# Kernel tuning notes

Measured on AMD Instinct MI355X. Metric: run time of the kernel, lower is better.

## Reference

```python
import jax, jax.numpy as jnp
import numpy as np

POOL = 4      # pool_size
SR = 2        # sampling_ratio (fixed; torchvision adaptive default approximated)
C_IN = 1024
C1, C2 = 256, 128
OUT_DIM = 2048


def setup_inputs() -> dict:
    key = jax.random.key(0)
    ks = jax.random.split(key, 10)
    B, C, H, W = 8, C_IN, 64, 64
    N = 64
    x = jax.random.normal(ks[0], (B, C, H, W), dtype=jnp.float32)
    # boxes in image pixel coords (image is H*16 = 1024 px)
    img = 1024.0
    x1 = jax.random.uniform(ks[1], (B, N), minval=0.0, maxval=img - 260.0)
    y1 = jax.random.uniform(ks[2], (B, N), minval=0.0, maxval=img - 260.0)
    bw = jax.random.uniform(ks[3], (B, N), minval=32.0, maxval=256.0)
    bh = jax.random.uniform(ks[4], (B, N), minval=32.0, maxval=256.0)
    boxes = jnp.stack([x1, y1, x1 + bw, y1 + bh], axis=-1)  # [B,N,4]
    scale = jnp.float32(1.0 / 16.0)
    # detector params
    w1 = jax.random.normal(ks[5], (C1, C_IN), dtype=jnp.float32) / np.sqrt(C_IN)
    b1 = jnp.zeros((C1,), dtype=jnp.float32)
    w2 = jax.random.normal(ks[6], (C2, C1), dtype=jnp.float32) / np.sqrt(C1)
    b2 = jnp.zeros((C2,), dtype=jnp.float32)
    wl = jax.random.normal(ks[7], (OUT_DIM, C2 * POOL * POOL), dtype=jnp.float32) / np.sqrt(C2 * POOL * POOL)
    bl = jnp.zeros((OUT_DIM,), dtype=jnp.float32)
    return {"x": x, "boxes": boxes, "scale": scale,
            "w1": w1, "b1": b1, "w2": w2, "b2": b2, "wl": wl, "bl": bl}


def _axis_coords(start, size, H):
    # start,size: [R]; returns coords [R, POOL*SR], valid mask, int low/high, lerp wts
    bin_sz = size / POOL                       # [R]
    j = jnp.arange(POOL * SR, dtype=jnp.float32)
    off = jnp.floor(j / SR) + ((j % SR) + 0.5) / SR   # [P]
    c = start[:, None] + off[None, :] * bin_sz[:, None]  # [R,P]
    valid = (c >= -1.0) & (c <= H)
    c = jnp.clip(c, 0.0, H - 1.0)
    lo = jnp.floor(c).astype(jnp.int32)
    lo = jnp.minimum(lo, H - 1)
    hi = jnp.minimum(lo + 1, H - 1)
    frac = c - lo.astype(c.dtype)
    return valid, lo, hi, frac


def _roi_align(feat, boxes, scale):
    # feat: [B,C,H,W], boxes: [B,N,4] -> pooled [B*N, C, POOL, POOL]
    B, C, H, W = feat.shape
    N = boxes.shape[1]
    R = B * N
    bx = (boxes.reshape(R, 4) * scale)
    x1, y1, x2, y2 = bx[:, 0], bx[:, 1], bx[:, 2], bx[:, 3]
    rw = jnp.maximum(x2 - x1, 1.0)
    rh = jnp.maximum(y2 - y1, 1.0)
    vy, y_lo, y_hi, ly = _axis_coords(y1, rh, H)   # [R,P]
    vx, x_lo, x_hi, lx = _axis_coords(x1, rw, W)
    hy, hx = 1.0 - ly, 1.0 - lx
    bidx = jnp.repeat(jnp.arange(B, dtype=jnp.int32), N)  # [R]
    b = bidx[:, None, None]
    # gather 4 corners -> [R,P,P,C]
    v00 = feat[b, :, y_lo[:, :, None], x_lo[:, None, :]]
    v01 = feat[b, :, y_lo[:, :, None], x_hi[:, None, :]]
    v10 = feat[b, :, y_hi[:, :, None], x_lo[:, None, :]]
    v11 = feat[b, :, y_hi[:, :, None], x_hi[:, None, :]]
    w00 = (hy[:, :, None] * hx[:, None, :])[..., None]
    w01 = (hy[:, :, None] * lx[:, None, :])[..., None]
    w10 = (ly[:, :, None] * hx[:, None, :])[..., None]
    w11 = (ly[:, :, None] * lx[:, None, :])[..., None]
    val = v00 * w00 + v01 * w01 + v10 * w10 + v11 * w11
    mask = (vy[:, :, None] & vx[:, None, :])[..., None]
    val = jnp.where(mask, val, 0.0)            # [R,P,P,C]
    val = val.reshape(R, POOL, SR, POOL, SR, C).mean(axis=(2, 4))  # [R,POOL,POOL,C]
    return jnp.transpose(val, (0, 3, 1, 2))    # [R,C,POOL,POOL]


def reference(x, boxes, scale, w1, b1, w2, b2, wl, bl):
    pooled = _roi_align(x, boxes, scale)                  # [R,C,4,4]
    h = jax.nn.elu(jnp.einsum('rchw,oc->rohw', pooled, w1) + b1[None, :, None, None])
    h = jax.nn.elu(jnp.einsum('rchw,oc->rohw', h, w2) + b2[None, :, None, None])
    h = h.reshape(h.shape[0], -1)                         # [R, 128*16], torch Flatten order
    out = jax.nn.elu(h @ wl.T + bl)                       # [R, 2048]
    return out
```

## Files before the change

kernel.cpp:

```cpp
#include <hip/hip_runtime.h>
#include <math.h>

#define C_INK   1024
#define C1D     256
#define C2D     128
#define OUTD    2048
#define R_ROI   512
#define M1D     8192
#define MPIX    32768

typedef _Float16 half8 __attribute__((ext_vector_type(8)));
typedef float    f32x4 __attribute__((ext_vector_type(4)));

__device__ __forceinline__ unsigned int pack2h(float a, float b) {
    union { _Float16 h[2]; unsigned int u; } p;
    p.h[0] = (_Float16)a; p.h[1] = (_Float16)b;
    return p.u;
}
__device__ __forceinline__ float eluf(float v) { return v > 0.f ? v : expf(v) - 1.f; }

template<int RC>
__device__ __forceinline__ half8* ldsq(_Float16* base, int row, int ch) {
    return reinterpret_cast<half8*>(base) + row * RC + (ch ^ (row & 7));
}

__global__ __launch_bounds__(256) void cvt_weights(
    const float* __restrict__ s1, _Float16* __restrict__ d1, int n1,
    const float* __restrict__ s2, _Float16* __restrict__ d2, int n2,
    const float* __restrict__ s3, _Float16* __restrict__ d3, int n3)
{
    int i = (blockIdx.x * 256 + threadIdx.x) * 4;
    const float* s; _Float16* d;
    if (i < n1)            { s = s1; d = d1; }
    else if (i < n1 + n2)  { s = s2; d = d2; i -= n1; }
    else                   { s = s3; d = d3; i -= n1 + n2; if (i >= n3) return; }
    const float4 v = *reinterpret_cast<const float4*>(s + i);
    uint2 u; u.x = pack2h(v.x, v.y); u.y = pack2h(v.z, v.w);
    *reinterpret_cast<uint2*>(d + i) = u;
}

__global__ __launch_bounds__(512, 4) void conv1x1_f16(
    const float* __restrict__ x, const _Float16* __restrict__ w1h,
    _Float16* __restrict__ z)
{
    __shared__ __align__(16) _Float16 As[64 * 64];
    __shared__ __align__(16) _Float16 Bs[256 * 64];

    const int tid  = threadIdx.x;
    const int lane = tid & 63;
    const int wave = tid >> 6;
    const int m0   = blockIdx.x * 64;
    const int b    = m0 >> 12;
    const int p0   = m0 & 4095;

    const int bc  = tid & 7;
    const int br0 = tid >> 3;

    float ar[8];
    half8 brg[4];
    f32x4 acc[4][2];
    #pragma unroll
    for (int i = 0; i < 4; ++i)
        #pragma unroll
        for (int j = 0; j < 2; ++j) acc[i][j] = (f32x4){0.f, 0.f, 0.f, 0.f};

    const float* xbase = x + (size_t)b * C_INK * 4096 + p0 + lane;

    auto LOADT = [&](int k0) {
        const float* xk = xbase + (size_t)(k0 + wave * 8) * 4096;
        #pragma unroll
        for (int j = 0; j < 8; ++j) ar[j] = xk[(size_t)j * 4096];
        #pragma unroll
        for (int i = 0; i < 4; ++i)
            brg[i] = *reinterpret_cast<const half8*>(
                &w1h[(size_t)(br0 + i * 64) * C_INK + k0 + bc * 8]);
    };
    auto WRITET = [&]() {
        union { half8 h; unsigned int u[4]; } pk;
        #pragma unroll
        for (int j = 0; j < 4; ++j) pk.u[j] = pack2h(ar[2 * j], ar[2 * j + 1]);
        *ldsq<8>(As, lane, wave) = pk.h;
        #pragma unroll
        for (int i = 0; i < 4; ++i) *ldsq<8>(Bs, br0 + i * 64, bc) = brg[i];
    };
    auto COMPUTET = [&]() {
        #pragma unroll
        for (int kk = 0; kk < 2; ++kk) {
            const int ch = kk * 4 + (lane >> 4);
            half8 af[4], bf[2];
            #pragma unroll
            for (int mi = 0; mi < 4; ++mi) af[mi] = *ldsq<8>(As, mi * 16 + (lane & 15), ch);
            #pragma unroll
            for (int ni = 0; ni < 2; ++ni) bf[ni] = *ldsq<8>(Bs, wave * 32 + ni * 16 + (lane & 15), ch);
            #pragma unroll
            for (int mi = 0; mi < 4; ++mi)
                #pragma unroll
                for (int ni = 0; ni < 2; ++ni)
                    acc[mi][ni] = __builtin_amdgcn_mfma_f32_16x16x32_f16(af[mi], bf[ni], acc[mi][ni], 0, 0, 0);
        }
    };

    LOADT(0); WRITET(); __syncthreads();
    for (int t = 0; t < 15; ++t) {
        LOADT((t + 1) * 64);
        COMPUTET();
        __syncthreads();
        WRITET();
        __syncthreads();
    }
    COMPUTET();

    _Float16* zp = z + (size_t)m0 * C1D;
    #pragma unroll
    for (int mi = 0; mi < 4; ++mi)
        #pragma unroll
        for (int ni = 0; ni < 2; ++ni)
            #pragma unroll
            for (int j = 0; j < 4; ++j) {
                const int row = mi * 16 + (lane >> 4) * 4 + j;
                const int col = wave * 32 + ni * 16 + (lane & 15);
                zp[(size_t)row * C1D + col] = (_Float16)acc[mi][ni][j];
            }
}

__global__ __launch_bounds__(256) void roi_gemm2_f16(
    const _Float16* __restrict__ z, const float* __restrict__ boxes,
    const float* __restrict__ scale_p, const float* __restrict__ b1v,
    const _Float16* __restrict__ w2h, const float* __restrict__ b2v,
    _Float16* __restrict__ h2)
{
    __shared__ __align__(16) _Float16 W2s[128 * 256];
    __shared__ __align__(16) _Float16 H1s[16 * 256];
    __shared__ int   s_off[64][4];
    __shared__ float s_w[64][4];

    const int r    = blockIdx.x;
    const int tid  = threadIdx.x;
    const int lane = tid & 63;

    if (tid < 64) {
        const float sc = scale_p[0];
        const float x1 = boxes[r * 4 + 0] * sc, y1 = boxes[r * 4 + 1] * sc;
        const float x2 = boxes[r * 4 + 2] * sc, y2 = boxes[r * 4 + 3] * sc;
        const float rw = fmaxf(x2 - x1, 1.f), rh = fmaxf(y2 - y1, 1.f);
        const int jy = tid >> 3, jx = tid & 7;

        float offy = (float)(jy >> 1) + (float)(jy & 1) * 0.5f + 0.25f;
        float cy = y1 + offy * rh * 0.25f;
        const bool vy = (cy >= -1.f) && (cy <= 64.f);
        cy = fminf(fmaxf(cy, 0.f), 63.f);
        int ylo = (int)cy; if (ylo > 63) ylo = 63;
        int yhi = ylo + 1; if (yhi > 63) yhi = 63;
        const float ly = cy - (float)ylo, hy = 1.f - ly;

        float offx = (float)(jx >> 1) + (float)(jx & 1) * 0.5f + 0.25f;
        float cx = x1 + offx * rw * 0.25f;
        const bool vx = (cx >= -1.f) && (cx <= 64.f);
        cx = fminf(fmaxf(cx, 0.f), 63.f);
        int xlo = (int)cx; if (xlo > 63) xlo = 63;
        int xhi = xlo + 1; if (xhi > 63) xhi = 63;
        const float lx = cx - (float)xlo, hx = 1.f - lx;

        const float wm = (vy && vx) ? 0.25f : 0.f;
        s_w[tid][0] = hy * hx * wm;
        s_w[tid][1] = hy * lx * wm;
        s_w[tid][2] = ly * hx * wm;
        s_w[tid][3] = ly * lx * wm;
        s_off[tid][0] = (ylo * 64 + xlo) * C1D;
        s_off[tid][1] = (ylo * 64 + xhi) * C1D;
        s_off[tid][2] = (yhi * 64 + xlo) * C1D;
        s_off[tid][3] = (yhi * 64 + xhi) * C1D;
    }

    {
        const int wr_ = tid >> 1;
        const int wcb = (tid & 1) * 16;
        #pragma unroll
        for (int bb = 0; bb < 4; ++bb) {
            half8 tmp[4];
            #pragma unroll
            for (int i = 0; i < 4; ++i)
                tmp[i] = *reinterpret_cast<const half8*>(&w2h[(size_t)wr_ * C1D + (wcb + bb * 4 + i) * 8]);
            #pragma unroll
            for (int i = 0; i < 4; ++i)
                *ldsq<32>(W2s, wr_, wcb + bb * 4 + i) = tmp[i];
        }
    }
    __syncthreads();

    {
        const int ch8 = tid & 31;
        const int cg  = tid >> 5;
        const _Float16* zb = z + (size_t)(r >> 6) * 4096 * C1D + ch8 * 8;

        float bias[8];
        {
            const float4 b0 = *reinterpret_cast<const float4*>(&b1v[ch8 * 8]);
            const float4 b4 = *reinterpret_cast<const float4*>(&b1v[ch8 * 8 + 4]);
            bias[0] = b0.x; bias[1] = b0.y; bias[2] = b0.z; bias[3] = b0.w;
            bias[4] = b4.x; bias[5] = b4.y; bias[6] = b4.z; bias[7] = b4.w;
        }

        float accv[2][8];
        #pragma unroll
        for (int c = 0; c < 2; ++c)
            #pragma unroll
            for (int e = 0; e < 8; ++e) accv[c][e] = 0.f;

        #pragma unroll
        for (int cc = 0; cc < 2; ++cc) {
            const int cell = cg * 2 + cc;
            const int py = cell >> 2, px = cell & 3;
            #pragma unroll
            for (int u = 0; u < 4; ++u) {
                const int s = (py * 2 + (u >> 1)) * 8 + px * 2 + (u & 1);
                #pragma unroll
                for (int k = 0; k < 4; ++k) {
                    const half8 v = *reinterpret_cast<const half8*>(zb + s_off[s][k]);
                    const float w = s_w[s][k];
                    #pragma unroll
                    for (int e = 0; e < 8; ++e) accv[cc][e] += (float)v[e] * w;
                }
            }
        }

        #pragma unroll
        for (int cc = 0; cc < 2; ++cc) {
            half8 o;
            #pragma unroll
            for (int e = 0; e < 8; ++e) o[e] = (_Float16)eluf(accv[cc][e] + bias[e]);
            *ldsq<32>(H1s, cg * 2 + cc, ch8) = o;
        }
    }
    __syncthreads();

    {
        const int wv = tid >> 6;
        f32x4 o2[2];
        o2[0] = (f32x4){0.f, 0.f, 0.f, 0.f};
        o2[1] = (f32x4){0.f, 0.f, 0.f, 0.f};

        #pragma unroll
        for (int ks = 0; ks < 8; ++ks) {
            const int ch = ks * 4 + (lane >> 4);
            const half8 af = *ldsq<32>(H1s, lane & 15, ch);
            #pragma unroll
            for (int i = 0; i < 2; ++i) {
                const half8 bf = *ldsq<32>(W2s, (wv * 2 + i) * 16 + (lane & 15), ch);
                o2[i] = __builtin_amdgcn_mfma_f32_16x16x32_f16(af, bf, o2[i], 0, 0, 0);
            }
        }

        _Float16* hp = h2 + (size_t)r * 2048;
        #pragma unroll
        for (int i = 0; i < 2; ++i) {
            const int o = (wv * 2 + i) * 16 + (lane & 15);
            const float bv = b2v[o];
            #pragma unroll
            for (int j = 0; j < 4; ++j) {
                const int p = (lane >> 4) * 4 + j;
                hp[o * 16 + p] = (_Float16)eluf(o2[i][j] + bv);
            }
        }
    }
}

template<int BM, int FM>
__global__ __launch_bounds__(256) void gemm_nt(
    const _Float16* __restrict__ A, const _Float16* __restrict__ W,
    const float* __restrict__ bias, float* __restrict__ Cout, int K, int N)
{
    constexpr int WM = FM * 16;
    constexpr int AI = BM / 32;
    __shared__ __align__(16) _Float16 As[BM * 64];
    __shared__ __align__(16) _Float16 Bs[128 * 64];

    const int tid  = threadIdx.x;
    const int lane = tid & 63;
    const int wave = tid >> 6;
    const int wr   = wave >> 1, wc = wave & 1;
    const int m0   = blockIdx.x * BM;
    const int n0   = blockIdx.y * 128;
    const int c    = tid & 7;
    const int r0   = tid >> 3;

    half8 arg[AI], brg[4];
    f32x4 acc[FM][4];
    #pragma unroll
    for (int i = 0; i < FM; ++i)
        #pragma unroll
        for (int j = 0; j < 4; ++j) acc[i][j] = (f32x4){0.f, 0.f, 0.f, 0.f};

    auto LOADT = [&](int k0) {
        #pragma unroll
        for (int i = 0; i < AI; ++i)
            arg[i] = *reinterpret_cast<const half8*>(&A[(size_t)(m0 + r0 + i * 32) * K + k0 + c * 8]);
        #pragma unroll
        for (int i = 0; i < 4; ++i)
            brg[i] = *reinterpret_cast<const half8*>(&W[(size_t)(n0 + r0 + i * 32) * K + k0 + c * 8]);
    };
    auto WRITET = [&]() {
        #pragma unroll
        for (int i = 0; i < AI; ++i) *ldsq<8>(As, r0 + i * 32, c) = arg[i];
        #pragma unroll
        for (int i = 0; i < 4; ++i)  *ldsq<8>(Bs, r0 + i * 32, c) = brg[i];
    };
    auto COMPUTET = [&]() {
        #pragma unroll
        for (int kk = 0; kk < 2; ++kk) {
            const int ch = kk * 4 + (lane >> 4);
            half8 af[FM], bf[4];
            #pragma unroll
            for (int mi = 0; mi < FM; ++mi) af[mi] = *ldsq<8>(As, wr * WM + mi * 16 + (lane & 15), ch);
            #pragma unroll
            for (int ni = 0; ni < 4; ++ni)  bf[ni] = *ldsq<8>(Bs, wc * 64 + ni * 16 + (lane & 15), ch);
            #pragma unroll
            for (int mi = 0; mi < FM; ++mi)
                #pragma unroll
                for (int ni = 0; ni < 4; ++ni)
                    acc[mi][ni] = __builtin_amdgcn_mfma_f32_16x16x32_f16(af[mi], bf[ni], acc[mi][ni], 0, 0, 0);
        }
    };

    const int nt = K / 64;
    LOADT(0); WRITET(); __syncthreads();
    for (int t = 0; t < nt - 1; ++t) {
        LOADT((t + 1) * 64);
        COMPUTET();
        __syncthreads();
        WRITET();
        __syncthreads();
    }
    COMPUTET();

    #pragma unroll
    for (int ni = 0; ni < 4; ++ni) {
        const int col = n0 + wc * 64 + ni * 16 + (lane & 15);
        const float bv = bias[col];
        #pragma unroll
        for (int mi = 0; mi < FM; ++mi)
            #pragma unroll
            for (int j = 0; j < 4; ++j) {
                const int row = m0 + wr * WM + mi * 16 + (lane >> 4) * 4 + j;
                Cout[(size_t)row * N + col] = eluf(acc[mi][ni][j] + bv);
            }
    }
}

extern "C" void kernel_launch(void* const* d_in, const int* in_sizes, int n_in,
                              void* d_out, int out_size, void* d_ws, size_t ws_size,
                              hipStream_t stream) {
    const float* x     = (const float*)d_in[0];
    const float* boxes = (const float*)d_in[1];
    const float* scale = (const float*)d_in[2];
    const float* w1    = (const float*)d_in[3];
    const float* b1    = (const float*)d_in[4];
    const float* w2    = (const float*)d_in[5];
    const float* b2    = (const float*)d_in[6];
    const float* wl    = (const float*)d_in[7];
    const float* bl    = (const float*)d_in[8];
    float* out = (float*)d_out;

    _Float16* z   = (_Float16*)d_ws;
    _Float16* h2  = z   + (size_t)MPIX * C1D;
    _Float16* w1h = h2  + (size_t)R_ROI * OUTD;
    _Float16* w2h = w1h + (size_t)C1D * C_INK;
    _Float16* wlh = w2h + (size_t)C2D * C1D;

    const int n1 = C1D * C_INK, n2 = C2D * C1D, n3 = OUTD * OUTD;

    cvt_weights<<<dim3((n1 + n2 + n3) / 1024), dim3(256), 0, stream>>>(
        w1, w1h, n1, w2, w2h, n2, wl, wlh, n3);

    conv1x1_f16<<<dim3(MPIX / 64), dim3(512), 0, stream>>>(x, w1h, z);

    roi_gemm2_f16<<<dim3(R_ROI), dim3(256), 0, stream>>>(
        z, boxes, scale, b1, w2h, b2, h2);

    gemm_nt<64, 2><<<dim3(R_ROI / 64, OUTD / 128), dim3(256), 0, stream>>>(
        h2, wlh, bl, out, OUTD, OUTD);
}
```

Measured before the change: 80.64 us.

## Restructure ROI and output GEMM kernels with 512 threads, register weights, vector stores

```diff
diff --git a/kernel.cpp b/kernel.cpp
--- a/kernel.cpp
+++ b/kernel.cpp
@@ -6,7 +6,6 @@
 #define C2D     128
 #define OUTD    2048
 #define R_ROI   512
-#define M1D     8192
 #define MPIX    32768
 
 typedef _Float16 half8 __attribute__((ext_vector_type(8)));
@@ -96,7 +95,7 @@
             for (int mi = 0; mi < 4; ++mi)
                 #pragma unroll
                 for (int ni = 0; ni < 2; ++ni)
-                    acc[mi][ni] = __builtin_amdgcn_mfma_f32_16x16x32_f16(af[mi], bf[ni], acc[mi][ni], 0, 0, 0);
+                    acc[mi][ni] = __builtin_amdgcn_mfma_f32_16x16x32_f16(bf[ni], af[mi], acc[mi][ni], 0, 0, 0);
         }
     };
 
@@ -112,31 +111,42 @@
 
     _Float16* zp = z + (size_t)m0 * C1D;
     #pragma unroll
-    for (int mi = 0; mi < 4; ++mi)
-        #pragma unroll
-        for (int ni = 0; ni < 2; ++ni)
-            #pragma unroll
-            for (int j = 0; j < 4; ++j) {
-                const int row = mi * 16 + (lane >> 4) * 4 + j;
-                const int col = wave * 32 + ni * 16 + (lane & 15);
-                zp[(size_t)row * C1D + col] = (_Float16)acc[mi][ni][j];
-            }
-}
-
-__global__ __launch_bounds__(256) void roi_gemm2_f16(
+    for (int mi = 0; mi < 4; ++mi) {
+        const int pixel = mi * 16 + (lane & 15);
+        #pragma unroll
+        for (int ni = 0; ni < 2; ++ni) {
+            const int oc0 = wave * 32 + ni * 16 + (lane >> 4) * 4;
+            uint2 u;
+            u.x = pack2h(acc[mi][ni][0], acc[mi][ni][1]);
+            u.y = pack2h(acc[mi][ni][2], acc[mi][ni][3]);
+            *reinterpret_cast<uint2*>(&zp[(size_t)pixel * C1D + oc0]) = u;
+        }
+    }
+}
+
+__global__ __launch_bounds__(512) void roi_gemm2_f16(
     const _Float16* __restrict__ z, const float* __restrict__ boxes,
     const float* __restrict__ scale_p, const float* __restrict__ b1v,
     const _Float16* __restrict__ w2h, const float* __restrict__ b2v,
     _Float16* __restrict__ h2)
 {
-    __shared__ __align__(16) _Float16 W2s[128 * 256];
     __shared__ __align__(16) _Float16 H1s[16 * 256];
     __shared__ int   s_off[64][4];
     __shared__ float s_w[64][4];
 
-    const int r    = blockIdx.x;
+    const int bid  = blockIdx.x;
+    const int r    = (bid & 7) * 64 + (bid >> 3);
     const int tid  = threadIdx.x;
     const int lane = tid & 63;
+    const int wv   = tid >> 6;
+
+    half8 bfr[8];
+    {
+        const _Float16* wp = w2h + (size_t)(wv * 16 + (lane & 15)) * C1D + (lane >> 4) * 8;
+        #pragma unroll
+        for (int ks = 0; ks < 8; ++ks)
+            bfr[ks] = *reinterpret_cast<const half8*>(wp + ks * 32);
+    }
 
     if (tid < 64) {
         const float sc = scale_p[0];
@@ -171,158 +181,117 @@
         s_off[tid][2] = (yhi * 64 + xlo) * C1D;
         s_off[tid][3] = (yhi * 64 + xhi) * C1D;
     }
+    __syncthreads();
 
     {
-        const int wr_ = tid >> 1;
-        const int wcb = (tid & 1) * 16;
-        #pragma unroll
-        for (int bb = 0; bb < 4; ++bb) {
-            half8 tmp[4];
-            #pragma unroll
-            for (int i = 0; i < 4; ++i)
-                tmp[i] = *reinterpret_cast<const half8*>(&w2h[(size_t)wr_ * C1D + (wcb + bb * 4 + i) * 8]);
-            #pragma unroll
-            for (int i = 0; i < 4; ++i)
-                *ldsq<32>(W2s, wr_, wcb + bb * 4 + i) = tmp[i];
-        }
+        const int ch8  = tid & 31;
+        const int cell = tid >> 5;
+        const _Float16* zb = z + (size_t)(r >> 6) * 4096 * C1D + ch8 * 8;
+
+        float accv[8];
+        #pragma unroll
+        for (int e = 0; e < 8; ++e) accv[e] = 0.f;
+
+        const int py = cell >> 2, px = cell & 3;
+        #pragma unroll
+        for (int u = 0; u < 4; ++u) {
+            const int s = (py * 2 + (u >> 1)) * 8 + px * 2 + (u & 1);
+            #pragma unroll
+            for (int k = 0; k < 4; ++k) {
+                const half8 v = *reinterpret_cast<const half8*>(zb + s_off[s][k]);
+                const float w = s_w[s][k];
+                #pragma unroll
+                for (int e = 0; e < 8; ++e) accv[e] += (float)v[e] * w;
+            }
+        }
+
+        const float4 b0 = *reinterpret_cast<const float4*>(&b1v[ch8 * 8]);
+        const float4 b4 = *reinterpret_cast<const float4*>(&b1v[ch8 * 8 + 4]);
+        half8 o;
+        o[0] = (_Float16)eluf(accv[0] + b0.x); o[1] = (_Float16)eluf(accv[1] + b0.y);
+        o[2] = (_Float16)eluf(accv[2] + b0.z); o[3] = (_Float16)eluf(accv[3] + b0.w);
+        o[4] = (_Float16)eluf(accv[4] + b4.x); o[5] = (_Float16)eluf(accv[5] + b4.y);
+        o[6] = (_Float16)eluf(accv[6] + b4.z); o[7] = (_Float16)eluf(accv[7] + b4.w);
+        *ldsq<32>(H1s, cell, ch8) = o;
     }
     __syncthreads();
 
+    f32x4 oa = (f32x4){0.f, 0.f, 0.f, 0.f};
+    #pragma unroll
+    for (int ks = 0; ks < 8; ++ks) {
+        const int ch = ks * 4 + (lane >> 4);
+        const half8 af = *ldsq<32>(H1s, lane & 15, ch);
+        oa = __builtin_amdgcn_mfma_f32_16x16x32_f16(af, bfr[ks], oa, 0, 0, 0);
+    }
+
     {
-        const int ch8 = tid & 31;
-        const int cg  = tid >> 5;
-        const _Float16* zb = z + (size_t)(r >> 6) * 4096 * C1D + ch8 * 8;
-
-        float bias[8];
-        {
-            const float4 b0 = *reinterpret_cast<const float4*>(&b1v[ch8 * 8]);
-            const float4 b4 = *reinterpret_cast<const float4*>(&b1v[ch8 * 8 + 4]);
-            bias[0] = b0.x; bias[1] = b0.y; bias[2] = b0.z; bias[3] = b0.w;
-            bias[4] = b4.x; bias[5] = b4.y; bias[6] = b4.z; bias[7] = b4.w;
-        }
-
-        float accv[2][8];
-        #pragma unroll
-        for (int c = 0; c < 2; ++c)
-            #pragma unroll
-            for (int e = 0; e < 8; ++e) accv[c][e] = 0.f;
-
-        #pragma unroll
-        for (int cc = 0; cc < 2; ++cc) {
-            const int cell = cg * 2 + cc;
-            const int py = cell >> 2, px = cell & 3;
-            #pragma unroll
-            for (int u = 0; u < 4; ++u) {
-                const int s = (py * 2 + (u >> 1)) * 8 + px * 2 + (u & 1);
-                #pragma unroll
-                for (int k = 0; k < 4; ++k) {
-                    const half8 v = *reinterpret_cast<const half8*>(zb + s_off[s][k]);
-                    const float w = s_w[s][k];
-                    #pragma unroll
-                    for (int e = 0; e < 8; ++e) accv[cc][e] += (float)v[e] * w;
-                }
-            }
-        }
-
-        #pragma unroll
-        for (int cc = 0; cc < 2; ++cc) {
-            half8 o;
-            #pragma unroll
-            for (int e = 0; e < 8; ++e) o[e] = (_Float16)eluf(accv[cc][e] + bias[e]);
-            *ldsq<32>(H1s, cg * 2 + cc, ch8) = o;
-        }
-    }
-    __syncthreads();
-
-    {
-        const int wv = tid >> 6;
-        f32x4 o2[2];
-        o2[0] = (f32x4){0.f, 0.f, 0.f, 0.f};
-        o2[1] = (f32x4){0.f, 0.f, 0.f, 0.f};
-
-        #pragma unroll
-        for (int ks = 0; ks < 8; ++ks) {
-            const int ch = ks * 4 + (lane >> 4);
-            const half8 af = *ldsq<32>(H1s, lane & 15, ch);
-            #pragma unroll
-            for (int i = 0; i < 2; ++i) {
-                const half8 bf = *ldsq<32>(W2s, (wv * 2 + i) * 16 + (lane & 15), ch);
-                o2[i] = __builtin_amdgcn_mfma_f32_16x16x32_f16(af, bf, o2[i], 0, 0, 0);
-            }
-        }
-
-        _Float16* hp = h2 + (size_t)r * 2048;
-        #pragma unroll
-        for (int i = 0; i < 2; ++i) {
-            const int o = (wv * 2 + i) * 16 + (lane & 15);
-            const float bv = b2v[o];
-            #pragma unroll
-            for (int j = 0; j < 4; ++j) {
-                const int p = (lane >> 4) * 4 + j;
-                hp[o * 16 + p] = (_Float16)eluf(o2[i][j] + bv);
-            }
-        }
-    }
-}
-
-template<int BM, int FM>
-__global__ __launch_bounds__(256) void gemm_nt(
+        const int o  = wv * 16 + (lane & 15);
+        const int p0 = (lane >> 4) * 4;
+        const float bv = b2v[o];
+        uint2 u;
+        u.x = pack2h(eluf(oa[0] + bv), eluf(oa[1] + bv));
+        u.y = pack2h(eluf(oa[2] + bv), eluf(oa[3] + bv));
+        *reinterpret_cast<uint2*>(&h2[(size_t)r * 2048 + o * 16 + p0]) = u;
+    }
+}
+
+__global__ __launch_bounds__(512) void gemm_nt_out(
     const _Float16* __restrict__ A, const _Float16* __restrict__ W,
-    const float* __restrict__ bias, float* __restrict__ Cout, int K, int N)
+    const float* __restrict__ bias, float* __restrict__ Cout)
 {
-    constexpr int WM = FM * 16;
-    constexpr int AI = BM / 32;
-    __shared__ __align__(16) _Float16 As[BM * 64];
+    constexpr int K = OUTD, N = OUTD;
+    __shared__ __align__(16) _Float16 As[64 * 64];
     __shared__ __align__(16) _Float16 Bs[128 * 64];
+
+    const int bid  = blockIdx.x;
+    const int xcd  = bid & 7;
+    const int idx  = bid >> 3;
+    const int n0   = (xcd * 2 + (idx & 1)) * 128;
+    const int m0   = (idx >> 1) * 64;
 
     const int tid  = threadIdx.x;
     const int lane = tid & 63;
     const int wave = tid >> 6;
-    const int wr   = wave >> 1, wc = wave & 1;
-    const int m0   = blockIdx.x * BM;
-    const int n0   = blockIdx.y * 128;
+    const int wr   = wave >> 2, wc = wave & 3;
     const int c    = tid & 7;
     const int r0   = tid >> 3;
 
-    half8 arg[AI], brg[4];
-    f32x4 acc[FM][4];
-    #pragma unroll
-    for (int i = 0; i < FM; ++i)
-        #pragma unroll
-        for (int j = 0; j < 4; ++j) acc[i][j] = (f32x4){0.f, 0.f, 0.f, 0.f};
+    half8 arg, brg[2];
+    f32x4 acc[2][2];
+    #pragma unroll
+    for (int i = 0; i < 2; ++i)
+        #pragma unroll
+        for (int j = 0; j < 2; ++j) acc[i][j] = (f32x4){0.f, 0.f, 0.f, 0.f};
 
     auto LOADT = [&](int k0) {
-        #pragma unroll
-        for (int i = 0; i < AI; ++i)
-            arg[i] = *reinterpret_cast<const half8*>(&A[(size_t)(m0 + r0 + i * 32) * K + k0 + c * 8]);
-        #pragma unroll
-        for (int i = 0; i < 4; ++i)
-            brg[i] = *reinterpret_cast<const half8*>(&W[(size_t)(n0 + r0 + i * 32) * K + k0 + c * 8]);
+        arg = *reinterpret_cast<const half8*>(&A[(size_t)(m0 + r0) * K + k0 + c * 8]);
+        #pragma unroll
+        for (int i = 0; i < 2; ++i)
+            brg[i] = *reinterpret_cast<const half8*>(&W[(size_t)(n0 + r0 + i * 64) * K + k0 + c * 8]);
     };
     auto WRITET = [&]() {
-        #pragma unroll
-        for (int i = 0; i < AI; ++i) *ldsq<8>(As, r0 + i * 32, c) = arg[i];
-        #pragma unroll
-        for (int i = 0; i < 4; ++i)  *ldsq<8>(Bs, r0 + i * 32, c) = brg[i];
+        *ldsq<8>(As, r0, c) = arg;
+        #pragma unroll
+        for (int i = 0; i < 2; ++i) *ldsq<8>(Bs, r0 + i * 64, c) = brg[i];
     };
     auto COMPUTET = [&]() {
         #pragma unroll
         for (int kk = 0; kk < 2; ++kk) {
             const int ch = kk * 4 + (lane >> 4);
-            half8 af[FM], bf[4];
-            #pragma unroll
-            for (int mi = 0; mi < FM; ++mi) af[mi] = *ldsq<8>(As, wr * WM + mi * 16 + (lane & 15), ch);
-            #pragma unroll
-            for (int ni = 0; ni < 4; ++ni)  bf[ni] = *ldsq<8>(Bs, wc * 64 + ni * 16 + (lane & 15), ch);
-            #pragma unroll
-            for (int mi = 0; mi < FM; ++mi)
+            half8 af[2], bf[2];
+            #pragma unroll
+            for (int mi = 0; mi < 2; ++mi) af[mi] = *ldsq<8>(As, wr * 32 + mi * 16 + (lane & 15), ch);
+            #pragma unroll
+            for (int ni = 0; ni < 2; ++ni) bf[ni] = *ldsq<8>(Bs, wc * 32 + ni * 16 + (lane & 15), ch);
+            #pragma unroll
+            for (int mi = 0; mi < 2; ++mi)
                 #pragma unroll
-                for (int ni = 0; ni < 4; ++ni)
-                    acc[mi][ni] = __builtin_amdgcn_mfma_f32_16x16x32_f16(af[mi], bf[ni], acc[mi][ni], 0, 0, 0);
-        }
-    };
-
-    const int nt = K / 64;
+                for (int ni = 0; ni < 2; ++ni)
+                    acc[mi][ni] = __builtin_amdgcn_mfma_f32_16x16x32_f16(bf[ni], af[mi], acc[mi][ni], 0, 0, 0);
+        }
+    };
+
+    constexpr int nt = K / 64;
     LOADT(0); WRITET(); __syncthreads();
     for (int t = 0; t < nt - 1; ++t) {
         LOADT((t + 1) * 64);
@@ -334,16 +303,19 @@
     COMPUTET();
 
     #pragma unroll
-    for (int ni = 0; ni < 4; ++ni) {
-        const int col = n0 + wc * 64 + ni * 16 + (lane & 15);
-        const float bv = bias[col];
-        #pragma unroll
-        for (int mi = 0; mi < FM; ++mi)
-            #pragma unroll
-            for (int j = 0; j < 4; ++j) {
-                const int row = m0 + wr * WM + mi * 16 + (lane >> 4) * 4 + j;
-                Cout[(size_t)row * N + col] = eluf(acc[mi][ni][j] + bv);
-            }
+    for (int mi = 0; mi < 2; ++mi) {
+        const int row = m0 + wr * 32 + mi * 16 + (lane & 15);
+        #pragma unroll
+        for (int ni = 0; ni < 2; ++ni) {
+            const int col0 = n0 + wc * 32 + ni * 16 + (lane >> 4) * 4;
+            const float4 bv = *reinterpret_cast<const float4*>(&bias[col0]);
+            float4 o;
+            o.x = eluf(acc[mi][ni][0] + bv.x);
+            o.y = eluf(acc[mi][ni][1] + bv.y);
+            o.z = eluf(acc[mi][ni][2] + bv.z);
+            o.w = eluf(acc[mi][ni][3] + bv.w);
+            *reinterpret_cast<float4*>(&Cout[(size_t)row * N + col0]) = o;
+        }
     }
 }
 
@@ -374,9 +346,8 @@
 
     conv1x1_f16<<<dim3(MPIX / 64), dim3(512), 0, stream>>>(x, w1h, z);
 
-    roi_gemm2_f16<<<dim3(R_ROI), dim3(256), 0, stream>>>(
+    roi_gemm2_f16<<<dim3(R_ROI), dim3(512), 0, stream>>>(
         z, boxes, scale, b1, w2h, b2, h2);
 
-    gemm_nt<64, 2><<<dim3(R_ROI / 64, OUTD / 128), dim3(256), 0, stream>>>(
-        h2, wlh, bl, out, OUTD, OUTD);
-}
+    gemm_nt_out<<<dim3(128), dim3(512), 0, stream>>>(h2, wlh, bl, out);
+}
```

After: 77.65 us. 3.7% less time.
